# Kernel optimization log

Measured on AMD Instinct MI355X. Metric: run time of the kernel, lower is better.

## Reference

```python
import jax, jax.numpy as jnp
import numpy as np

B, C, H, W = 2, 512, 64, 64
NUM_GROUPS = 32
EPS = 1e-6


def setup_inputs() -> dict:
    key = jax.random.key(0)
    ks = jax.random.split(key, 6)
    s = 1.0 / np.sqrt(C)
    return {
        "x": jax.random.normal(ks[0], (B, C, H, W), dtype=jnp.float32),
        "gn_scale": jnp.ones((C,), jnp.float32),
        "gn_bias": jnp.zeros((C,), jnp.float32),
        "wq": jax.random.normal(ks[1], (C, C), jnp.float32) * s,
        "bq": jnp.zeros((C,), jnp.float32),
        "wk": jax.random.normal(ks[2], (C, C), jnp.float32) * s,
        "bk": jnp.zeros((C,), jnp.float32),
        "wv": jax.random.normal(ks[3], (C, C), jnp.float32) * s,
        "bv": jnp.zeros((C,), jnp.float32),
        "wp": jax.random.normal(ks[4], (C, C), jnp.float32) * s,
        "bp": jnp.zeros((C,), jnp.float32),
    }


def group_norm(x, scale, bias):
    # x: [b, c, h, w]; GroupNorm with NUM_GROUPS groups, eps=1e-6, affine
    b, c, h, w = x.shape
    xg = x.reshape(b, NUM_GROUPS, c // NUM_GROUPS, h, w)
    mean = jnp.mean(xg, axis=(2, 3, 4), keepdims=True)
    var = jnp.var(xg, axis=(2, 3, 4), keepdims=True)
    xg = (xg - mean) * jax.lax.rsqrt(var + EPS)
    xn = xg.reshape(b, c, h, w)
    return xn * scale[None, :, None, None] + bias[None, :, None, None]


def reference(x, gn_scale, gn_bias, wq, bq, wk, bk, wv, bv, wp, bp):
    b, c, h, w = x.shape
    n = h * w
    hn = group_norm(x, gn_scale, gn_bias).reshape(b, c, n)  # [b,c,n]
    # 1x1 convs == per-pixel linear over channels
    q = jnp.einsum('dc,bcn->bdn', wq, hn) + bq[None, :, None]
    k = jnp.einsum('dc,bcn->bdn', wk, hn) + bk[None, :, None]
    v = jnp.einsum('dc,bcn->bdn', wv, hn) + bv[None, :, None]
    # attn[b,i,j] = softmax_j( q[:, :, i] . k[:, :, j] / sqrt(c) )
    attn = jnp.einsum('bci,bcj->bij', q, k) * (float(c) ** -0.5)
    attn = jax.nn.softmax(attn, axis=-1)
    out = jnp.einsum('bcj,bij->bci', v, attn)  # [b,c,n]
    out = jnp.einsum('dc,bcn->bdn', wp, out) + bp[None, :, None]
    return x + out.reshape(b, c, h, w)
```

## Files before the change

### kernel.cpp

```cpp
#include <hip/hip_runtime.h>

typedef __bf16 bf16x8 __attribute__((ext_vector_type(8)));
typedef float f32x4 __attribute__((ext_vector_type(4)));
typedef int i32x8 __attribute__((ext_vector_type(8)));


#if defined(__has_builtin)
#if __has_builtin(__builtin_amdgcn_global_load_lds)
#define HAS_GLL 1
#endif
#endif

__device__ __forceinline__ void async_copy16(const void* g, void* l) {
#ifdef HAS_GLL
    __builtin_amdgcn_global_load_lds(
        (const __attribute__((address_space(1))) unsigned int*)g,
        (__attribute__((address_space(3))) unsigned int*)l, 16, 0, 0);
#else
    *(int4*)l = *(const int4*)g;
#endif
}

__device__ __forceinline__ unsigned char to_fp8(float v) {
    return (unsigned char)(__builtin_amdgcn_cvt_pk_fp8_f32(v, v, 0, false) & 0xFF);
}

#define MXSCALE 0x7F7F7F7F

__global__ __launch_bounds__(256) void prep_kernel(
    const float* __restrict__ x, float* __restrict__ ps,
    const float* __restrict__ wq, const float* __restrict__ wk,
    const float* __restrict__ wv, const float* __restrict__ wp,
    const float* __restrict__ bq, const float* __restrict__ bk,
    unsigned char* __restrict__ wqk8, unsigned char* __restrict__ wv8,
    __bf16* __restrict__ wp_b, float* __restrict__ bqk) {
    if (blockIdx.x >= 1024) {
        int idx = (blockIdx.x - 1024) * 256 + threadIdx.x;
        wqk8[idx] = to_fp8(wq[idx]);
        wqk8[262144 + idx] = to_fp8(wk[idx]);
        wv8[idx] = to_fp8(wv[idx]);
        wp_b[idx] = (__bf16)wp[idx];
        if (idx < 512) {
            bqk[idx] = bq[idx];
            bqk[512 + idx] = bk[idx];
        }
        return;
    }
    int blk = blockIdx.x;
    const float4* base = (const float4*)x + (size_t)blk * 1024;
    float s1 = 0.f, s2 = 0.f;
#pragma unroll
    for (int i = 0; i < 4; ++i) {
        float4 v = base[threadIdx.x + (i << 8)];
        s1 += v.x + v.y + v.z + v.w;
        s2 += v.x * v.x + v.y * v.y + v.z * v.z + v.w * v.w;
    }
    for (int off = 32; off >= 1; off >>= 1) {
        s1 += __shfl_xor(s1, off);
        s2 += __shfl_xor(s2, off);
    }
    __shared__ float r1[4], r2[4];
    int wave = threadIdx.x >> 6, lane = threadIdx.x & 63;
    if (lane == 0) { r1[wave] = s1; r2[wave] = s2; }
    __syncthreads();
    if (threadIdx.x == 0) {
        ps[blk] = r1[0] + r1[1] + r1[2] + r1[3];
        ps[1024 + blk] = r2[0] + r2[1] + r2[2] + r2[3];
    }
}

__global__ __launch_bounds__(256) void gn_apply_kernel(const float* __restrict__ x,
                                                       const float* __restrict__ gn_scale,
                                                       const float* __restrict__ gn_bias,
                                                       const float* __restrict__ ps,
                                                       unsigned char* __restrict__ hn8) {
    __shared__ float tile[32][33];
    int b = blockIdx.z;
    int n0 = blockIdx.x * 32, c0 = blockIdx.y * 32;
    int tx = threadIdx.x & 31, ty = threadIdx.x >> 5;
    const float* xb = x + (size_t)b * 512 * 4096;
#pragma unroll
    for (int r = 0; r < 4; ++r) {
        int c = ty + r * 8;
        tile[c][tx] = xb[(size_t)(c0 + c) * 4096 + n0 + tx];
    }
    int c = c0 + tx;
    int g = (b << 5) + (c >> 4);
    float s1 = 0.f, s2 = 0.f;
#pragma unroll
    for (int i = 0; i < 16; ++i) {
        s1 += ps[(g << 4) + i];
        s2 += ps[1024 + (g << 4) + i];
    }
    float m = s1 * (1.f / 65536.f);
    float var = s2 * (1.f / 65536.f) - m * m;
    float rs = rsqrtf(var + 1e-6f);
    float sc = gn_scale[c] * rs;
    float bi = gn_bias[c] - m * sc;
    __syncthreads();
    unsigned char* outp = hn8 + (size_t)b * 4096 * 512;
#pragma unroll
    for (int r = 0; r < 4; ++r) {
        int n = ty + r * 8;
        float v = tile[tx][n];
        outp[(size_t)(n0 + n) * 512 + c] = to_fp8(v * sc + bi);
    }
}

template <int BN, int OUT_MODE, int BIAS_MODE>
__device__ __forceinline__ void mx_gemm_body(
    const unsigned char* __restrict__ Ab, int lda,
    const unsigned char* __restrict__ Bb, int ldb,
    void* __restrict__ C, int ldc,
    const float* __restrict__ bias, int K, float scale,
    long m0, long n0, unsigned char* As, unsigned char* Bs) {
    constexpr int NT = BN / 32;
    const int tid = threadIdx.x;
    const int lane = tid & 63, wave = tid >> 6;
    const int ln = lane & 15, q = lane >> 4;
    const int wm = (wave >> 1) << 6;
    const int wn = (wave & 1) * (BN / 2);

    f32x4 acc[4][NT] = {};

    for (int k0 = 0; k0 < K; k0 += 128) {
        __syncthreads();
#pragma unroll
        for (int p = 0; p < 4; ++p) {
            int c = (p << 8) + tid;
            int row = c >> 3, sg = ((c & 7) ^ (row & 7)) << 4;
            async_copy16(Ab + (long)row * lda + k0 + sg, &As[c << 4]);
        }
#pragma unroll
        for (int p = 0; p < BN / 32; ++p) {
            int c = (p << 8) + tid;
            int row = c >> 3, sg = ((c & 7) ^ (row & 7)) << 4;
            async_copy16(Bb + (long)row * ldb + k0 + sg, &Bs[c << 4]);
        }
        __syncthreads();
        i32x8 af[4], bf[NT];
#pragma unroll
        for (int t = 0; t < 4; ++t) {
            int row = wm + t * 16 + ln, e = row & 7;
            const unsigned char* bp = &As[row << 7];
            *(int4*)&af[t] = *(const int4*)(bp + ((((q << 1)) ^ e) << 4));
            *((int4*)&af[t] + 1) = *(const int4*)(bp + ((((q << 1) | 1) ^ e) << 4));
        }
#pragma unroll
        for (int t = 0; t < NT; ++t) {
            int row = wn + t * 16 + ln, e = row & 7;
            const unsigned char* bp = &Bs[row << 7];
            *(int4*)&bf[t] = *(const int4*)(bp + ((((q << 1)) ^ e) << 4));
            *((int4*)&bf[t] + 1) = *(const int4*)(bp + ((((q << 1) | 1) ^ e) << 4));
        }
#pragma unroll
        for (int mt = 0; mt < 4; ++mt)
#pragma unroll
            for (int nt = 0; nt < NT; ++nt)
                acc[mt][nt] = __builtin_amdgcn_mfma_scale_f32_16x16x128_f8f6f4(
                    af[mt], bf[nt], acc[mt][nt], 0, 0, 0, MXSCALE, 0, MXSCALE);
    }

#pragma unroll
    for (int mt = 0; mt < 4; ++mt) {
#pragma unroll
        for (int nt = 0; nt < NT; ++nt) {
            long col = n0 + wn + nt * 16 + ln;
#pragma unroll
            for (int r = 0; r < 4; ++r) {
                long row = m0 + wm + mt * 16 + (q << 2) + r;
                float v = acc[mt][nt][r] * scale;
                if (BIAS_MODE == 1) v += bias[row];
                if (BIAS_MODE == 2) v += bias[col];
                long off = row * (long)ldc + col;
                if (OUT_MODE == 0) {
                    ((unsigned char*)C)[off] = to_fp8(v);
                } else {
                    ((_Float16*)C)[off] = (_Float16)v;
                }
            }
        }
    }
}

__global__ __launch_bounds__(256) void qkv_kernel(
    const unsigned char* __restrict__ hn8, const unsigned char* __restrict__ wqk8,
    const unsigned char* __restrict__ wv8, const float* __restrict__ bqk,
    const float* __restrict__ bv, unsigned char* __restrict__ qk8,
    unsigned char* __restrict__ v8) {
    __shared__ __align__(16) unsigned char As[128 * 128];
    __shared__ __align__(16) unsigned char Bs[128 * 128];
    int z = blockIdx.z;
    if (z < 2) {
        long b = z;
        long m0 = (long)blockIdx.y * 128, n0 = (long)blockIdx.x * 128;
        mx_gemm_body<128, 0, 2>(hn8 + b * 4096 * 512 + m0 * 512, 512,
                                wqk8 + n0 * 512, 512,
                                qk8 + b * 4096 * 1024, 1024,
                                bqk, 512, 1.f, m0, n0, As, Bs);
    } else {
        long b = z - 2;
        int flat = blockIdx.y * 8 + blockIdx.x;
        long m0 = (long)(flat >> 6) * 128, n0 = (long)(flat & 63) * 64;
        mx_gemm_body<64, 0, 1>(wv8 + m0 * 512, 512,
                               hn8 + b * 4096 * 512 + n0 * 512, 512,
                               v8 + b * 512 * 4096, 4096,
                               bv, 512, 1.f, m0, n0, As, Bs);
    }
}

__global__ __launch_bounds__(256) void mx_s_kernel(const unsigned char* __restrict__ QK,
                                                   unsigned char* __restrict__ S,
                                                   float scale) {
    __shared__ __align__(16) unsigned char As[128 * 128];
    __shared__ __align__(16) unsigned char Bs[128 * 128];
    long b = blockIdx.z;
    long m0 = (long)blockIdx.y * 128, n0 = (long)blockIdx.x * 128;
    mx_gemm_body<128, 0, 0>(QK + b * 4096 * 1024 + m0 * 1024, 1024,
                            QK + b * 4096 * 1024 + n0 * 1024 + 512, 1024,
                            S + b * 4096 * 4096, 4096,
                            nullptr, 512, scale, m0, n0, As, Bs);
}

#define CVT4(dst, base, word)                                   \
    dst[base + 0] = __builtin_amdgcn_cvt_f32_fp8(word, 0);      \
    dst[base + 1] = __builtin_amdgcn_cvt_f32_fp8(word, 1);      \
    dst[base + 2] = __builtin_amdgcn_cvt_f32_fp8(word, 2);      \
    dst[base + 3] = __builtin_amdgcn_cvt_f32_fp8(word, 3);

__global__ __launch_bounds__(256) void softmax_kernel(unsigned char* __restrict__ S) {
    long row = blockIdx.x;
    unsigned char* srow = S + (row << 12);
    int tid = threadIdx.x;
    int4 d = ((const int4*)srow)[tid];
    float v[16];
    CVT4(v, 0, d.x)
    CVT4(v, 4, d.y)
    CVT4(v, 8, d.z)
    CVT4(v, 12, d.w)
    float mx = -1e30f;
#pragma unroll
    for (int p = 0; p < 16; ++p) mx = fmaxf(mx, v[p]);
    for (int off = 32; off >= 1; off >>= 1) mx = fmaxf(mx, __shfl_xor(mx, off));
    __shared__ float red[4], red2[4];
    int wave = tid >> 6, lane = tid & 63;
    if (lane == 0) red[wave] = mx;
    __syncthreads();
    mx = fmaxf(fmaxf(red[0], red[1]), fmaxf(red[2], red[3]));
    float s = 0.f;
#pragma unroll
    for (int p = 0; p < 16; ++p) {
        v[p] = __expf(v[p] - mx);
        s += v[p];
    }
    for (int off = 32; off >= 1; off >>= 1) s += __shfl_xor(s, off);
    if (lane == 0) red2[wave] = s;
    __syncthreads();
    s = red2[0] + red2[1] + red2[2] + red2[3];
    float inv64 = 64.f / s;
    int w[4];
#pragma unroll
    for (int i = 0; i < 4; ++i) {
        w[i] = __builtin_amdgcn_cvt_pk_fp8_f32(v[4 * i] * inv64, v[4 * i + 1] * inv64, 0, false);
        w[i] = __builtin_amdgcn_cvt_pk_fp8_f32(v[4 * i + 2] * inv64, v[4 * i + 3] * inv64, w[i], true);
    }
    ((int4*)srow)[tid] = make_int4(w[0], w[1], w[2], w[3]);
}

__global__ __launch_bounds__(256) void mx_pv_kernel(const unsigned char* __restrict__ P,
                                                    const unsigned char* __restrict__ V,
                                                    __bf16* __restrict__ O) {
    __shared__ __align__(16) unsigned char As[128 * 128];
    __shared__ __align__(16) unsigned char Bs[64 * 128];
    const int tid = threadIdx.x;
    const int lane = tid & 63, wave = tid >> 6;
    const int ln = lane & 15, q = lane >> 4;
    const int wm = (wave >> 1) << 6, wn = (wave & 1) << 5;
    const int b = blockIdx.x >> 5;
    const long m0 = (long)(blockIdx.x & 31) * 128;
    const long n0 = (long)blockIdx.y * 64;
    const unsigned char* Pb = P + ((long)b * 4096 + m0) * 4096;
    const unsigned char* Vb = V + ((long)b * 512 + n0) * 4096;

    f32x4 acc[4][2] = {};

    for (int k0 = 0; k0 < 4096; k0 += 128) {
        __syncthreads();
#pragma unroll
        for (int p = 0; p < 4; ++p) {
            int c = (p << 8) + tid;
            int row = c >> 3, sg = ((c & 7) ^ (row & 7)) << 4;
            async_copy16(Pb + (long)row * 4096 + k0 + sg, &As[c << 4]);
        }
#pragma unroll
        for (int p = 0; p < 2; ++p) {
            int c = (p << 8) + tid;
            int row = c >> 3, sg = ((c & 7) ^ (row & 7)) << 4;
            async_copy16(Vb + (long)row * 4096 + k0 + sg, &Bs[c << 4]);
        }
        __syncthreads();
        i32x8 af[4], bf[2];
#pragma unroll
        for (int t = 0; t < 4; ++t) {
            int row = wm + t * 16 + ln, e = row & 7;
            const unsigned char* ap = &As[row << 7];
            *(int4*)&af[t] = *(const int4*)(ap + ((((q << 1)) ^ e) << 4));
            *((int4*)&af[t] + 1) = *(const int4*)(ap + ((((q << 1) | 1) ^ e) << 4));
        }
#pragma unroll
        for (int t = 0; t < 2; ++t) {
            int row = wn + t * 16 + ln, e = row & 7;
            const unsigned char* bp = &Bs[row << 7];
            *(int4*)&bf[t] = *(const int4*)(bp + ((((q << 1)) ^ e) << 4));
            *((int4*)&bf[t] + 1) = *(const int4*)(bp + ((((q << 1) | 1) ^ e) << 4));
        }
#pragma unroll
        for (int mt = 0; mt < 4; ++mt)
#pragma unroll
            for (int nt = 0; nt < 2; ++nt)
                acc[mt][nt] = __builtin_amdgcn_mfma_scale_f32_16x16x128_f8f6f4(
                    af[mt], bf[nt], acc[mt][nt], 0, 0, 0, MXSCALE, 0, MXSCALE);
    }

    __bf16* Ob = O + (long)b * 4096 * 512;
#pragma unroll
    for (int mt = 0; mt < 4; ++mt) {
#pragma unroll
        for (int nt = 0; nt < 2; ++nt) {
            long col = n0 + wn + nt * 16 + ln;
#pragma unroll
            for (int r = 0; r < 4; ++r) {
                long row = m0 + wm + mt * 16 + (q << 2) + r;
                Ob[row * 512 + col] = (__bf16)(acc[mt][nt][r] * 0.015625f);
            }
        }
    }
}

__global__ __launch_bounds__(256) void proj_kernel(
    const __bf16* __restrict__ A, const __bf16* __restrict__ Bt, long bsB,
    float* __restrict__ C, long bsC, const float* __restrict__ bias,
    const float* __restrict__ resid) {
    __shared__ __align__(16) __bf16 As[128][64];
    __shared__ __align__(16) __bf16 Bs[64][64];
    const int tid = threadIdx.x;
    const int wave = tid >> 6, lane = tid & 63;
    const int q = lane >> 4, ln = lane & 15;
    const int wm = wave << 5;
    const long m0 = (long)blockIdx.y * 128, n0 = (long)blockIdx.x * 64;
    const int b = blockIdx.z;
    const __bf16* Ab = A + m0 * 512;
    const __bf16* Bb = Bt + (long)b * bsB + n0 * 512;

    f32x4 acc[2][4] = {};

    for (int k0 = 0; k0 < 512; k0 += 64) {
        __syncthreads();
#pragma unroll
        for (int p = 0; p < 4; ++p) {
            int c = (p << 8) + tid;
            int row = c >> 3, sg = (c & 7) << 3;
            async_copy16(Ab + (long)row * 512 + k0 + sg, &As[0][0] + (c << 3));
        }
#pragma unroll
        for (int p = 0; p < 2; ++p) {
            int c = (p << 8) + tid;
            int row = c >> 3, sg = (c & 7) << 3;
            async_copy16(Bb + (long)row * 512 + k0 + sg, &Bs[0][0] + (c << 3));
        }
        __syncthreads();
#pragma unroll
        for (int kk = 0; kk < 2; ++kk) {
            bf16x8 af[2], bfr[4];
#pragma unroll
            for (int mt = 0; mt < 2; ++mt)
                af[mt] = *(const bf16x8*)(&As[wm + mt * 16 + ln][(kk << 5) + (q << 3)]);
#pragma unroll
            for (int nt = 0; nt < 4; ++nt)
                bfr[nt] = *(const bf16x8*)(&Bs[nt * 16 + ln][(kk << 5) + (q << 3)]);
#pragma unroll
            for (int mt = 0; mt < 2; ++mt)
#pragma unroll
                for (int nt = 0; nt < 4; ++nt)
                    acc[mt][nt] = __builtin_amdgcn_mfma_f32_16x16x32_bf16(
                        af[mt], bfr[nt], acc[mt][nt], 0, 0, 0);
        }
    }

#pragma unroll
    for (int mt = 0; mt < 2; ++mt) {
#pragma unroll
        for (int nt = 0; nt < 4; ++nt) {
            long col = n0 + nt * 16 + ln;
#pragma unroll
            for (int r = 0; r < 4; ++r) {
                long row = m0 + wm + mt * 16 + (q << 2) + r;
                long off = (long)b * bsC + row * 4096 + col;
                C[off] = acc[mt][nt][r] + bias[row] + resid[off];
            }
        }
    }
}

extern "C" void kernel_launch(void* const* d_in, const int* in_sizes, int n_in,
                              void* d_out, int out_size, void* d_ws, size_t ws_size,
                              hipStream_t stream) {
    const float* x = (const float*)d_in[0];
    const float* gn_scale = (const float*)d_in[1];
    const float* gn_bias = (const float*)d_in[2];
    const float* wq = (const float*)d_in[3];
    const float* bq = (const float*)d_in[4];
    const float* wk = (const float*)d_in[5];
    const float* bk = (const float*)d_in[6];
    const float* wv = (const float*)d_in[7];
    const float* bv = (const float*)d_in[8];
    const float* wp = (const float*)d_in[9];
    const float* bp = (const float*)d_in[10];
    float* out = (float*)d_out;

    char* ws = (char*)d_ws;
    unsigned char* wqk8 = (unsigned char*)(ws + 0x0);
    unsigned char* wv8 = (unsigned char*)(ws + 0x80000);
    __bf16* wp_b = (__bf16*)(ws + 0xC0000);
    float* bqk = (float*)(ws + 0x140000);
    float* psum = (float*)(ws + 0x142000);
    unsigned char* hn8 = (unsigned char*)(ws + 0x150000);
    unsigned char* qk8 = (unsigned char*)(ws + 0x550000);
    unsigned char* v8 = (unsigned char*)(ws + 0xD50000);
    __bf16* o_t = (__bf16*)(ws + 0x1150000);
    unsigned char* S8 = (unsigned char*)(ws + 0x1950000);
    (void)ws_size;

    prep_kernel<<<2048, 256, 0, stream>>>(x, psum, wq, wk, wv, wp, bq, bk,
                                          wqk8, wv8, wp_b, bqk);
    gn_apply_kernel<<<dim3(128, 16, 2), 256, 0, stream>>>(x, gn_scale, gn_bias,
                                                          psum, hn8);

    qkv_kernel<<<dim3(8, 32, 4), 256, 0, stream>>>(hn8, wqk8, wv8, bqk, bv,
                                                   qk8, v8);

    const float attn_scale = 0.044194173824159216f;
    mx_s_kernel<<<dim3(32, 32, 2), 256, 0, stream>>>(qk8, S8, attn_scale);
    softmax_kernel<<<8192, 256, 0, stream>>>(S8);
    mx_pv_kernel<<<dim3(64, 8), 256, 0, stream>>>(S8, v8, o_t);

    proj_kernel<<<dim3(64, 4, 2), 256, 0, stream>>>(
        wp_b, o_t, 4096l * 512, out, 512l * 4096, bp, x);
}
```

Baseline: 190.6 us.

## Double-buffer LDS tiles in MX fp8 GEMMs to overlap loads with MFMA

Adds double-buffered shared memory tiles to the shared GEMM body and to the PV kernel. The next K-tile is prefetched with async global-to-LDS copies while MFMAs run on the current tile, which also removes one barrier per iteration. The goal is to hide global load latency behind compute. In exchange, LDS use per block doubles (up to 64KB), which can cut the number of resident blocks per CU. If the compiler inserts a full vmcnt wait before the LDS reads, the intended overlap may be lost.

Measured after the change: 191.8 us. Within noise of the previous version (+0.6%).

```diff
diff --git a/kernel.cpp b/kernel.cpp
--- a/kernel.cpp
+++ b/kernel.cpp
@@ -115,6 +115,7 @@
     const float* __restrict__ bias, int K, float scale,
     long m0, long n0, unsigned char* As, unsigned char* Bs) {
     constexpr int NT = BN / 32;
+    constexpr int BSZ = BN * 128;
     const int tid = threadIdx.x;
     const int lane = tid & 63, wave = tid >> 6;
     const int ln = lane & 15, q = lane >> 4;
@@ -123,33 +124,54 @@
 
     f32x4 acc[4][NT] = {};
 
-    for (int k0 = 0; k0 < K; k0 += 128) {
+#pragma unroll
+    for (int p = 0; p < 4; ++p) {
+        int c = (p << 8) + tid;
+        int row = c >> 3, sg = ((c & 7) ^ (row & 7)) << 4;
+        async_copy16(Ab + (long)row * lda + sg, &As[c << 4]);
+    }
+#pragma unroll
+    for (int p = 0; p < NT; ++p) {
+        int c = (p << 8) + tid;
+        int row = c >> 3, sg = ((c & 7) ^ (row & 7)) << 4;
+        async_copy16(Bb + (long)row * ldb + sg, &Bs[c << 4]);
+    }
+
+    const int nk = K >> 7;
+    for (int ki = 0; ki < nk; ++ki) {
         __syncthreads();
-#pragma unroll
-        for (int p = 0; p < 4; ++p) {
-            int c = (p << 8) + tid;
-            int row = c >> 3, sg = ((c & 7) ^ (row & 7)) << 4;
-            async_copy16(Ab + (long)row * lda + k0 + sg, &As[c << 4]);
-        }
-#pragma unroll
-        for (int p = 0; p < BN / 32; ++p) {
-            int c = (p << 8) + tid;
-            int row = c >> 3, sg = ((c & 7) ^ (row & 7)) << 4;
-            async_copy16(Bb + (long)row * ldb + k0 + sg, &Bs[c << 4]);
-        }
-        __syncthreads();
+        const int cur = ki & 1;
+        if (ki + 1 < nk) {
+            const int k1 = (ki + 1) << 7;
+            unsigned char* Ad = As + (cur ^ 1) * 16384;
+            unsigned char* Bd = Bs + (cur ^ 1) * BSZ;
+#pragma unroll
+            for (int p = 0; p < 4; ++p) {
+                int c = (p << 8) + tid;
+                int row = c >> 3, sg = ((c & 7) ^ (row & 7)) << 4;
+                async_copy16(Ab + (long)row * lda + k1 + sg, Ad + (c << 4));
+            }
+#pragma unroll
+            for (int p = 0; p < NT; ++p) {
+                int c = (p << 8) + tid;
+                int row = c >> 3, sg = ((c & 7) ^ (row & 7)) << 4;
+                async_copy16(Bb + (long)row * ldb + k1 + sg, Bd + (c << 4));
+            }
+        }
+        const unsigned char* Ar = As + cur * 16384;
+        const unsigned char* Br = Bs + cur * BSZ;
         i32x8 af[4], bf[NT];
 #pragma unroll
         for (int t = 0; t < 4; ++t) {
             int row = wm + t * 16 + ln, e = row & 7;
-            const unsigned char* bp = &As[row << 7];
-            *(int4*)&af[t] = *(const int4*)(bp + ((((q << 1)) ^ e) << 4));
-            *((int4*)&af[t] + 1) = *(const int4*)(bp + ((((q << 1) | 1) ^ e) << 4));
+            const unsigned char* ap = Ar + (row << 7);
+            *(int4*)&af[t] = *(const int4*)(ap + ((((q << 1)) ^ e) << 4));
+            *((int4*)&af[t] + 1) = *(const int4*)(ap + ((((q << 1) | 1) ^ e) << 4));
         }
 #pragma unroll
         for (int t = 0; t < NT; ++t) {
             int row = wn + t * 16 + ln, e = row & 7;
-            const unsigned char* bp = &Bs[row << 7];
+            const unsigned char* bp = Br + (row << 7);
             *(int4*)&bf[t] = *(const int4*)(bp + ((((q << 1)) ^ e) << 4));
             *((int4*)&bf[t] + 1) = *(const int4*)(bp + ((((q << 1) | 1) ^ e) << 4));
         }
@@ -188,8 +210,8 @@
     const unsigned char* __restrict__ wv8, const float* __restrict__ bqk,
     const float* __restrict__ bv, unsigned char* __restrict__ qk8,
     unsigned char* __restrict__ v8) {
-    __shared__ __align__(16) unsigned char As[128 * 128];
-    __shared__ __align__(16) unsigned char Bs[128 * 128];
+    __shared__ __align__(16) unsigned char As[2 * 128 * 128];
+    __shared__ __align__(16) unsigned char Bs[2 * 128 * 128];
     int z = blockIdx.z;
     if (z < 2) {
         long b = z;
@@ -212,8 +234,8 @@
 __global__ __launch_bounds__(256) void mx_s_kernel(const unsigned char* __restrict__ QK,
                                                    unsigned char* __restrict__ S,
                                                    float scale) {
-    __shared__ __align__(16) unsigned char As[128 * 128];
-    __shared__ __align__(16) unsigned char Bs[128 * 128];
+    __shared__ __align__(16) unsigned char As[2 * 128 * 128];
+    __shared__ __align__(16) unsigned char Bs[2 * 128 * 128];
     long b = blockIdx.z;
     long m0 = (long)blockIdx.y * 128, n0 = (long)blockIdx.x * 128;
     mx_gemm_body<128, 0, 0>(QK + b * 4096 * 1024 + m0 * 1024, 1024,
@@ -270,8 +292,8 @@
 __global__ __launch_bounds__(256) void mx_pv_kernel(const unsigned char* __restrict__ P,
                                                     const unsigned char* __restrict__ V,
                                                     __bf16* __restrict__ O) {
-    __shared__ __align__(16) unsigned char As[128 * 128];
-    __shared__ __align__(16) unsigned char Bs[64 * 128];
+    __shared__ __align__(16) unsigned char As[2 * 128 * 128];
+    __shared__ __align__(16) unsigned char Bs[2 * 64 * 128];
     const int tid = threadIdx.x;
     const int lane = tid & 63, wave = tid >> 6;
     const int ln = lane & 15, q = lane >> 4;
@@ -284,33 +306,53 @@
 
     f32x4 acc[4][2] = {};
 
-    for (int k0 = 0; k0 < 4096; k0 += 128) {
+#pragma unroll
+    for (int p = 0; p < 4; ++p) {
+        int c = (p << 8) + tid;
+        int row = c >> 3, sg = ((c & 7) ^ (row & 7)) << 4;
+        async_copy16(Pb + (long)row * 4096 + sg, &As[c << 4]);
+    }
+#pragma unroll
+    for (int p = 0; p < 2; ++p) {
+        int c = (p << 8) + tid;
+        int row = c >> 3, sg = ((c & 7) ^ (row & 7)) << 4;
+        async_copy16(Vb + (long)row * 4096 + sg, &Bs[c << 4]);
+    }
+
+    for (int ki = 0; ki < 32; ++ki) {
         __syncthreads();
-#pragma unroll
-        for (int p = 0; p < 4; ++p) {
-            int c = (p << 8) + tid;
-            int row = c >> 3, sg = ((c & 7) ^ (row & 7)) << 4;
-            async_copy16(Pb + (long)row * 4096 + k0 + sg, &As[c << 4]);
-        }
-#pragma unroll
-        for (int p = 0; p < 2; ++p) {
-            int c = (p << 8) + tid;
-            int row = c >> 3, sg = ((c & 7) ^ (row & 7)) << 4;
-            async_copy16(Vb + (long)row * 4096 + k0 + sg, &Bs[c << 4]);
-        }
-        __syncthreads();
+        const int cur = ki & 1;
+        if (ki + 1 < 32) {
+            const int k1 = (ki + 1) << 7;
+            unsigned char* Ad = As + (cur ^ 1) * 16384;
+            unsigned char* Bd = Bs + (cur ^ 1) * 8192;
+#pragma unroll
+            for (int p = 0; p < 4; ++p) {
+                int c = (p << 8) + tid;
+                int row = c >> 3, sg = ((c & 7) ^ (row & 7)) << 4;
+                async_copy16(Pb + (long)row * 4096 + k1 + sg, Ad + (c << 4));
+            }
+#pragma unroll
+            for (int p = 0; p < 2; ++p) {
+                int c = (p << 8) + tid;
+                int row = c >> 3, sg = ((c & 7) ^ (row & 7)) << 4;
+                async_copy16(Vb + (long)row * 4096 + k1 + sg, Bd + (c << 4));
+            }
+        }
+        const unsigned char* Ar = As + cur * 16384;
+        const unsigned char* Br = Bs + cur * 8192;
         i32x8 af[4], bf[2];
 #pragma unroll
         for (int t = 0; t < 4; ++t) {
             int row = wm + t * 16 + ln, e = row & 7;
-            const unsigned char* ap = &As[row << 7];
+            const unsigned char* ap = Ar + (row << 7);
             *(int4*)&af[t] = *(const int4*)(ap + ((((q << 1)) ^ e) << 4));
             *((int4*)&af[t] + 1) = *(const int4*)(ap + ((((q << 1) | 1) ^ e) << 4));
         }
 #pragma unroll
         for (int t = 0; t < 2; ++t) {
             int row = wn + t * 16 + ln, e = row & 7;
-            const unsigned char* bp = &Bs[row << 7];
+            const unsigned char* bp = Br + (row << 7);
             *(int4*)&bf[t] = *(const int4*)(bp + ((((q << 1)) ^ e) << 4));
             *((int4*)&bf[t] + 1) = *(const int4*)(bp + ((((q << 1) | 1) ^ e) << 4));
         }
```

## Double-buffer LDS in MX-FP8 GEMM body and route PV kernel through it

Applied to the files above, without the earlier changes.

Turns the shared FP8 MFMA GEMM loop into a two-stage LDS pipeline. Tile k+2 is issued asynchronously while tile k is computed, using explicit vmcnt/lgkmcnt waits and raw barriers instead of two __syncthreads per iteration. MFMA issue priority is raised with s_setprio. The PV kernel now reuses the shared body through a new bf16 output mode. LDS use doubles (up to 64KB per block), which may cut occupancy, and the hand-counted vmcnt values must match the number of outstanding loads exactly.

Measured after the change: 184.9 us. 3.0% less time.

```diff
diff --git a/kernel.cpp b/kernel.cpp
--- a/kernel.cpp
+++ b/kernel.cpp
@@ -26,6 +26,9 @@
 }
 
 #define MXSCALE 0x7F7F7F7F
+
+#define ASM_VMCNT(N) asm volatile("s_waitcnt vmcnt(" #N ")" ::: "memory")
+#define ASM_LGKM0() asm volatile("s_waitcnt lgkmcnt(0)" ::: "memory")
 
 __global__ __launch_bounds__(256) void prep_kernel(
     const float* __restrict__ x, float* __restrict__ ps,
@@ -115,6 +118,7 @@
     const float* __restrict__ bias, int K, float scale,
     long m0, long n0, unsigned char* As, unsigned char* Bs) {
     constexpr int NT = BN / 32;
+    constexpr int BSZ = BN * 128;
     const int tid = threadIdx.x;
     const int lane = tid & 63, wave = tid >> 6;
     const int ln = lane & 15, q = lane >> 4;
@@ -123,42 +127,65 @@
 
     f32x4 acc[4][NT] = {};
 
-    for (int k0 = 0; k0 < K; k0 += 128) {
-        __syncthreads();
+    auto stage = [&](int kt, int buf) {
+        const int k0 = kt << 7;
+        unsigned char* Ad = As + buf * 16384;
+        unsigned char* Bd = Bs + buf * BSZ;
 #pragma unroll
         for (int p = 0; p < 4; ++p) {
             int c = (p << 8) + tid;
             int row = c >> 3, sg = ((c & 7) ^ (row & 7)) << 4;
-            async_copy16(Ab + (long)row * lda + k0 + sg, &As[c << 4]);
-        }
-#pragma unroll
-        for (int p = 0; p < BN / 32; ++p) {
+            async_copy16(Ab + (long)row * lda + k0 + sg, Ad + (c << 4));
+        }
+#pragma unroll
+        for (int p = 0; p < NT; ++p) {
             int c = (p << 8) + tid;
             int row = c >> 3, sg = ((c & 7) ^ (row & 7)) << 4;
-            async_copy16(Bb + (long)row * ldb + k0 + sg, &Bs[c << 4]);
-        }
-        __syncthreads();
+            async_copy16(Bb + (long)row * ldb + k0 + sg, Bd + (c << 4));
+        }
+    };
+
+    const int nk = K >> 7;
+    stage(0, 0);
+    if (nk > 1) stage(1, 1);
+
+    for (int ki = 0; ki < nk; ++ki) {
+        if (ki < nk - 1) {
+            if constexpr (NT == 4) ASM_VMCNT(8);
+            else ASM_VMCNT(6);
+        } else {
+            ASM_VMCNT(0);
+        }
+        __builtin_amdgcn_s_barrier();
+        const int cur = ki & 1;
+        const unsigned char* Ar = As + cur * 16384;
+        const unsigned char* Br = Bs + cur * BSZ;
         i32x8 af[4], bf[NT];
 #pragma unroll
         for (int t = 0; t < 4; ++t) {
             int row = wm + t * 16 + ln, e = row & 7;
-            const unsigned char* bp = &As[row << 7];
-            *(int4*)&af[t] = *(const int4*)(bp + ((((q << 1)) ^ e) << 4));
-            *((int4*)&af[t] + 1) = *(const int4*)(bp + ((((q << 1) | 1) ^ e) << 4));
+            const unsigned char* ap = Ar + (row << 7);
+            *(int4*)&af[t] = *(const int4*)(ap + ((((q << 1)) ^ e) << 4));
+            *((int4*)&af[t] + 1) = *(const int4*)(ap + ((((q << 1) | 1) ^ e) << 4));
         }
 #pragma unroll
         for (int t = 0; t < NT; ++t) {
             int row = wn + t * 16 + ln, e = row & 7;
-            const unsigned char* bp = &Bs[row << 7];
+            const unsigned char* bp = Br + (row << 7);
             *(int4*)&bf[t] = *(const int4*)(bp + ((((q << 1)) ^ e) << 4));
             *((int4*)&bf[t] + 1) = *(const int4*)(bp + ((((q << 1) | 1) ^ e) << 4));
         }
+        ASM_LGKM0();
+        __builtin_amdgcn_s_barrier();
+        if (ki + 2 < nk) stage(ki + 2, cur);
+        __builtin_amdgcn_s_setprio(1);
 #pragma unroll
         for (int mt = 0; mt < 4; ++mt)
 #pragma unroll
             for (int nt = 0; nt < NT; ++nt)
                 acc[mt][nt] = __builtin_amdgcn_mfma_scale_f32_16x16x128_f8f6f4(
                     af[mt], bf[nt], acc[mt][nt], 0, 0, 0, MXSCALE, 0, MXSCALE);
+        __builtin_amdgcn_s_setprio(0);
     }
 
 #pragma unroll
@@ -175,8 +202,10 @@
                 long off = row * (long)ldc + col;
                 if (OUT_MODE == 0) {
                     ((unsigned char*)C)[off] = to_fp8(v);
+                } else if (OUT_MODE == 1) {
+                    ((_Float16*)C)[off] = (_Float16)v;
                 } else {
-                    ((_Float16*)C)[off] = (_Float16)v;
+                    ((__bf16*)C)[off] = (__bf16)v;
                 }
             }
         }
@@ -188,8 +217,8 @@
     const unsigned char* __restrict__ wv8, const float* __restrict__ bqk,
     const float* __restrict__ bv, unsigned char* __restrict__ qk8,
     unsigned char* __restrict__ v8) {
-    __shared__ __align__(16) unsigned char As[128 * 128];
-    __shared__ __align__(16) unsigned char Bs[128 * 128];
+    __shared__ __align__(16) unsigned char As[2 * 128 * 128];
+    __shared__ __align__(16) unsigned char Bs[2 * 128 * 128];
     int z = blockIdx.z;
     if (z < 2) {
         long b = z;
@@ -212,8 +241,8 @@
 __global__ __launch_bounds__(256) void mx_s_kernel(const unsigned char* __restrict__ QK,
                                                    unsigned char* __restrict__ S,
                                                    float scale) {
-    __shared__ __align__(16) unsigned char As[128 * 128];
-    __shared__ __align__(16) unsigned char Bs[128 * 128];
+    __shared__ __align__(16) unsigned char As[2 * 128 * 128];
+    __shared__ __align__(16) unsigned char Bs[2 * 128 * 128];
     long b = blockIdx.z;
     long m0 = (long)blockIdx.y * 128, n0 = (long)blockIdx.x * 128;
     mx_gemm_body<128, 0, 0>(QK + b * 4096 * 1024 + m0 * 1024, 1024,
@@ -270,71 +299,15 @@
 __global__ __launch_bounds__(256) void mx_pv_kernel(const unsigned char* __restrict__ P,
                                                     const unsigned char* __restrict__ V,
                                                     __bf16* __restrict__ O) {
-    __shared__ __align__(16) unsigned char As[128 * 128];
-    __shared__ __align__(16) unsigned char Bs[64 * 128];
-    const int tid = threadIdx.x;
-    const int lane = tid & 63, wave = tid >> 6;
-    const int ln = lane & 15, q = lane >> 4;
-    const int wm = (wave >> 1) << 6, wn = (wave & 1) << 5;
+    __shared__ __align__(16) unsigned char As[2 * 128 * 128];
+    __shared__ __align__(16) unsigned char Bs[2 * 64 * 128];
     const int b = blockIdx.x >> 5;
     const long m0 = (long)(blockIdx.x & 31) * 128;
     const long n0 = (long)blockIdx.y * 64;
-    const unsigned char* Pb = P + ((long)b * 4096 + m0) * 4096;
-    const unsigned char* Vb = V + ((long)b * 512 + n0) * 4096;
-
-    f32x4 acc[4][2] = {};
-
-    for (int k0 = 0; k0 < 4096; k0 += 128) {
-        __syncthreads();
-#pragma unroll
-        for (int p = 0; p < 4; ++p) {
-            int c = (p << 8) + tid;
-            int row = c >> 3, sg = ((c & 7) ^ (row & 7)) << 4;
-            async_copy16(Pb + (long)row * 4096 + k0 + sg, &As[c << 4]);
-        }
-#pragma unroll
-        for (int p = 0; p < 2; ++p) {
-            int c = (p << 8) + tid;
-            int row = c >> 3, sg = ((c & 7) ^ (row & 7)) << 4;
-            async_copy16(Vb + (long)row * 4096 + k0 + sg, &Bs[c << 4]);
-        }
-        __syncthreads();
-        i32x8 af[4], bf[2];
-#pragma unroll
-        for (int t = 0; t < 4; ++t) {
-            int row = wm + t * 16 + ln, e = row & 7;
-            const unsigned char* ap = &As[row << 7];
-            *(int4*)&af[t] = *(const int4*)(ap + ((((q << 1)) ^ e) << 4));
-            *((int4*)&af[t] + 1) = *(const int4*)(ap + ((((q << 1) | 1) ^ e) << 4));
-        }
-#pragma unroll
-        for (int t = 0; t < 2; ++t) {
-            int row = wn + t * 16 + ln, e = row & 7;
-            const unsigned char* bp = &Bs[row << 7];
-            *(int4*)&bf[t] = *(const int4*)(bp + ((((q << 1)) ^ e) << 4));
-            *((int4*)&bf[t] + 1) = *(const int4*)(bp + ((((q << 1) | 1) ^ e) << 4));
-        }
-#pragma unroll
-        for (int mt = 0; mt < 4; ++mt)
-#pragma unroll
-            for (int nt = 0; nt < 2; ++nt)
-                acc[mt][nt] = __builtin_amdgcn_mfma_scale_f32_16x16x128_f8f6f4(
-                    af[mt], bf[nt], acc[mt][nt], 0, 0, 0, MXSCALE, 0, MXSCALE);
-    }
-
-    __bf16* Ob = O + (long)b * 4096 * 512;
-#pragma unroll
-    for (int mt = 0; mt < 4; ++mt) {
-#pragma unroll
-        for (int nt = 0; nt < 2; ++nt) {
-            long col = n0 + wn + nt * 16 + ln;
-#pragma unroll
-            for (int r = 0; r < 4; ++r) {
-                long row = m0 + wm + mt * 16 + (q << 2) + r;
-                Ob[row * 512 + col] = (__bf16)(acc[mt][nt][r] * 0.015625f);
-            }
-        }
-    }
+    mx_gemm_body<64, 2, 0>(P + ((long)b * 4096 + m0) * 4096, 4096,
+                           V + ((long)b * 512 + n0) * 4096, 4096,
+                           O + (long)b * 4096 * 512, 512,
+                           nullptr, 4096, 0.015625f, m0, n0, As, Bs);
 }
 
 __global__ __launch_bounds__(256) void proj_kernel(
```
